# Optimization experiments

Hardware: AMD Instinct MI355X
Metric: run time of the kernel (lower is better)

Reference implementation:

```python
import jax, jax.numpy as jnp
import numpy as np

W_KERNEL = 5      # dilation kernel size (w)
K_BG = 0.1        # background weight (k)
RELAX = 5.0       # sigmoid temperature (relax)
INF = 1e4         # 'no zero in column' sentinel (>> image diagonal)
EPS = 1e-7        # DiceLoss eps


def setup_inputs() -> dict:
    key = jax.random.key(0)
    k1, k2 = jax.random.split(key)
    B, H, W = 32, 256, 256
    preds = jax.random.normal(k1, (B, H, W), dtype=jnp.float32)
    targets = (jax.random.uniform(k2, (B, H, W)) > 0.99).astype(jnp.float32)
    return {"preds": preds, "targets": targets}


def _dilate(t, w):
    # cv2.dilate with w x w ones kernel == sliding-window max, SAME padding
    pad = w // 2
    return jax.lax.reduce_window(t, -jnp.inf, jax.lax.max,
                                 (1, w, w), (1, 1, 1),
                                 [(0, 0), (pad, pad), (pad, pad)])


def _vertical_dist(zero_mask):
    # per-column distance (in rows) to nearest zero pixel; [B,H,W] -> [B,H,W]
    B, H, W = zero_mask.shape
    rows = jnp.moveaxis(zero_mask, 1, 0)  # [H,B,W]

    def step(carry, z):
        d = jnp.where(z, 0.0, jnp.minimum(carry + 1.0, INF))
        return d, d

    init = jnp.full((B, W), INF, dtype=jnp.float32)
    _, fwd = jax.lax.scan(step, init, rows)
    _, bwd = jax.lax.scan(step, init, rows[::-1])
    g = jnp.minimum(fwd, bwd[::-1])  # [H,B,W]
    return jnp.moveaxis(g, 0, 1)


def _edt(fat):
    # exact euclidean distance transform (distance to nearest zero pixel),
    # separable two-pass: vertical 1D distance, then horizontal min-plus.
    B, H, W = fat.shape
    g = _vertical_dist(fat == 0)  # [B,H,W]
    col = jnp.arange(W, dtype=jnp.float32)
    off2 = (col[:, None] - col[None, :]) ** 2  # [W_j, W_k]

    def per_img(gi):  # gi: [H,W]
        # d2[i,j] = min_k g[i,k]^2 + (j-k)^2   -> [H,W,W] intermediate
        d2 = jnp.min(gi[:, None, :] ** 2 + off2[None, :, :], axis=-1)
        return jnp.sqrt(d2)

    return jax.lax.map(per_img, g)  # sequential over batch caps memory


def _distance_maps(targets):
    fat = _dilate(targets, W_KERNEL)          # [B,H,W]
    d = _edt(fat)                              # [B,H,W]
    soft = jax.nn.sigmoid(d / RELAX)
    soft = soft - jnp.min(soft, axis=(1, 2), keepdims=True)
    mx = jnp.max(soft, axis=(1, 2), keepdims=True)
    soft = soft / jnp.where(mx > 0, mx, 1.0)
    dm_soft = soft + (1.0 - fat) * K_BG
    has_fg = jnp.max(targets, axis=(1, 2), keepdims=True) > 0
    return jnp.where(has_fg, dm_soft, 1.0 - targets)


def reference(preds, targets):
    p = jax.nn.sigmoid(preds)
    dm = jax.lax.stop_gradient(_distance_maps(targets))  # computed in numpy in torch => constant
    pw = p * dm
    bs = pw.shape[0]
    y_pred = pw.reshape(bs, 1, -1)
    y_true = targets.reshape(bs, 1, -1)
    # smp DiceLoss('binary', from_logits=False): dims=(0,2), smooth=0, eps=1e-7
    inter = jnp.sum(y_pred * y_true, axis=(0, 2))
    card = jnp.sum(y_pred + y_true, axis=(0, 2))
    dice = (2.0 * inter) / jnp.maximum(card, EPS)
    loss = 1.0 - dice
    mask = (jnp.sum(y_true, axis=(0, 2)) > 0).astype(loss.dtype)
    return jnp.mean(loss * mask)
```

## Files before the change

kernel.cpp:

```cpp
#include <hip/hip_runtime.h>
#include <math.h>

#define BB 32
#define HH 256
#define WW 256
#define HW (HH*WW)
#define K_BG 0.1f
#define RELAX 5.0f
#define EPS_D 1e-7
#define RPB 8

typedef unsigned long long u64;
typedef unsigned short u16;

__device__ __forceinline__ float sigf(float x) { return 1.0f / (1.0f + expf(-x)); }

__device__ __forceinline__ u64 shflx64(u64 x, int s) {
    return (u64)__shfl_xor((unsigned long long)x, s, 64);
}

__global__ void k_maskdil(const float* __restrict__ tg, u64* __restrict__ dmaskT,
                          u64* __restrict__ nzmask) {
    __shared__ u64 nz[20][4];
    __shared__ u64 hd[20][4];
    int blk = blockIdx.x;
    int b = blk >> 4, band = blk & 15;
    int r0 = band * 16;
    int t = threadIdx.x, w = t >> 6;
    const float* img = tg + b * HW;
    float v[20];
    #pragma unroll
    for (int rr = 0; rr < 20; ++rr) {
        int rg = r0 + rr - 2;
        v[rr] = (rg >= 0 && rg < HH) ? img[rg * WW + t] : 0.0f;
    }
    #pragma unroll
    for (int rr = 0; rr < 20; ++rr) {
        u64 bal = __ballot(v[rr] != 0.0f);
        if ((t & 63) == 0) nz[rr][w] = bal;
    }
    __syncthreads();
    if (t < 80) {
        int rr = t >> 2, k = t & 3;
        u64 m = nz[rr][k];
        u64 ml = (k > 0) ? nz[rr][k - 1] : 0ULL;
        u64 mr = (k < 3) ? nz[rr][k + 1] : 0ULL;
        hd[rr][k] = m | (m << 1) | (m << 2) | (m >> 1) | (m >> 2)
                  | (ml >> 62) | (ml >> 63) | (mr << 62) | (mr << 63);
    }
    if (t < 64) {
        int rr = t >> 2, k = t & 3;
        nzmask[b * 1024 + (r0 + rr) * 4 + k] = nz[rr + 2][k];
    }
    __syncthreads();
    if (t < 64) {
        int rr = t >> 2, k = t & 3;
        u64 o = hd[rr][k] | hd[rr + 1][k] | hd[rr + 2][k] | hd[rr + 3][k] | hd[rr + 4][k];
        dmaskT[b * 1024 + k * 256 + (r0 + rr)] = o;
    }
}

__global__ __launch_bounds__(256) void k_mega(const float* __restrict__ preds,
                                              const u64* __restrict__ dmaskT,
                                              const u64* __restrict__ nzmask,
                                              float4* __restrict__ part1,
                                              float4* __restrict__ part2) {
    __shared__ u64 colT[4 * 256];
    __shared__ u16 gS[RPB][WW];
    __shared__ float red[8][4];
    int blk = blockIdx.x;
    int b = blk >> 5, q = blk & 31;
    int i0 = q * RPB;
    int tid = threadIdx.x;
    int lane = tid & 63, wv = tid >> 6;
    int j = tid;

    float p[RPB];
    #pragma unroll
    for (int rr = 0; rr < RPB; ++rr)
        p[rr] = preds[(b * HH + i0 + rr) * WW + j];
    u64 nzw[RPB];
    #pragma unroll
    for (int rr = 0; rr < RPB; ++rr)
        nzw[rr] = nzmask[b * 1024 + (i0 + rr) * 4 + wv];

    const u64* base = dmaskT + b * 1024;
    const u64 L32 = 0x00000000FFFFFFFFULL, L16 = 0x0000FFFF0000FFFFULL,
              L8  = 0x00FF00FF00FF00FFULL, L4  = 0x0F0F0F0F0F0F0F0FULL,
              L2  = 0x3333333333333333ULL, L1  = 0x5555555555555555ULL;
    #pragma unroll
    for (int w = 0; w < 4; ++w) {
        u64 x = base[w * 256 + wv * 64 + lane];
        u64 pp;
        pp = shflx64(x, 32); x = (lane & 32) ? ((x & ~L32) | ((pp & ~L32) >> 32)) : ((x & L32) | ((pp & L32) << 32));
        pp = shflx64(x, 16); x = (lane & 16) ? ((x & ~L16) | ((pp & ~L16) >> 16)) : ((x & L16) | ((pp & L16) << 16));
        pp = shflx64(x,  8); x = (lane &  8) ? ((x & ~L8 ) | ((pp & ~L8 ) >>  8)) : ((x & L8 ) | ((pp & L8 ) <<  8));
        pp = shflx64(x,  4); x = (lane &  4) ? ((x & ~L4 ) | ((pp & ~L4 ) >>  4)) : ((x & L4 ) | ((pp & L4 ) <<  4));
        pp = shflx64(x,  2); x = (lane &  2) ? ((x & ~L2 ) | ((pp & ~L2 ) >>  2)) : ((x & L2 ) | ((pp & L2 ) <<  2));
        pp = shflx64(x,  1); x = (lane &  1) ? ((x & ~L1 ) | ((pp & ~L1 ) >>  1)) : ((x & L1 ) | ((pp & L1 ) <<  1));
        colT[wv * 256 + w * 64 + lane] = x;
    }
    __syncthreads();

    u64 yw[4];
    #pragma unroll
    for (int g = 0; g < 4; ++g) yw[g] = ~colT[g * 256 + j];

    int g0v[RPB], fgv[RPB];
    #pragma unroll
    for (int rr = 0; rr < RPB; ++rr) {
        int i = i0 + rr;
        int iw = i >> 6, ib = i & 63;
        u64 lowm  = (2ULL << ib) - 1ULL;
        u64 highm = ~((1ULL << ib) - 1ULL);
        int pu = -1, pd = -1;
        #pragma unroll
        for (int w = 0; w < 4; ++w) {
            u64 m = (w < iw) ? ~0ULL : ((w == iw) ? lowm : 0ULL);
            u64 z = yw[w] & m;
            int cand = (w << 6) + 63 - __clzll(z);
            pu = z ? cand : pu;
        }
        #pragma unroll
        for (int w = 3; w >= 0; --w) {
            u64 m = (w > iw) ? ~0ULL : ((w == iw) ? highm : 0ULL);
            u64 z = yw[w] & m;
            int cand = (w << 6) + (__ffsll((unsigned long long)z) - 1);
            pd = z ? cand : pd;
        }
        int up = (pu >= 0) ? (i - pu) : 10000;
        int dn = (pd >= 0) ? (pd - i) : 10000;
        int g0 = min(min(up, dn), 10000);
        g0v[rr] = g0;
        fgv[rr] = (int)((~yw[iw] >> ib) & 1ULL);
        gS[rr][j] = (u16)g0;
    }
    __syncthreads();

    float vals[8];
    #pragma unroll
    for (int qq = 0; qq < 6; ++qq) vals[qq] = 0.0f;
    vals[6] = 1e30f; vals[7] = 0.0f;
    #pragma unroll
    for (int rr = 0; rr < RPB; ++rr) {
        float gv = (float)g0v[rr];
        float best = gv * gv;
        #pragma unroll
        for (int r = 1; r <= 8; ++r) {
            float rf = (float)(r * r);
            int jl = j - r, jr = j + r;
            float vl = (jl >= 0) ? (float)gS[rr][jl] : 1e4f;
            float vr = (jr < WW) ? (float)gS[rr][jr] : 1e4f;
            best = fminf(best, fminf(fmaf(vl, vl, rf), fmaf(vr, vr, rf)));
        }
        for (int rc = 9; rc < WW + 8; rc += 8) {
            if ((float)(rc * rc) >= best) break;
            #pragma unroll
            for (int dr = 0; dr < 8; ++dr) {
                int r = rc + dr;
                float rf = (float)(r * r);
                int jl = j - r, jr = j + r;
                float vl = (jl >= 0) ? (float)gS[rr][jl] : 1e4f;
                float vr = (jr < WW) ? (float)gS[rr][jr] : 1e4f;
                best = fminf(best, fminf(fmaf(vl, vl, rf), fmaf(vr, vr, rf)));
            }
        }
        float dv = sqrtf(best);
        float sp = sigf(p[rr]);
        float sd = sigf(dv / RELAX);
        float tv = (float)((nzw[rr] >> (j & 63)) & 1ULL);
        vals[0] += sp * sd * tv;
        vals[1] += sp * tv;
        vals[2] += sp * sd;
        vals[3] += sp;
        vals[4] += fgv[rr] ? 0.0f : sp;
        vals[5] += tv;
        vals[6] = fminf(vals[6], dv);
        vals[7] = fmaxf(vals[7], dv);
    }
    for (int off = 32; off > 0; off >>= 1) {
        #pragma unroll
        for (int qq = 0; qq < 6; ++qq) vals[qq] += __shfl_down(vals[qq], off, 64);
        vals[6] = fminf(vals[6], __shfl_down(vals[6], off, 64));
        vals[7] = fmaxf(vals[7], __shfl_down(vals[7], off, 64));
    }
    if (lane == 0) {
        #pragma unroll
        for (int qq = 0; qq < 8; ++qq) red[qq][wv] = vals[qq];
    }
    __syncthreads();
    if (tid == 0) {
        float s[8];
        #pragma unroll
        for (int qq = 0; qq < 6; ++qq) s[qq] = red[qq][0] + red[qq][1] + red[qq][2] + red[qq][3];
        s[6] = fminf(fminf(red[6][0], red[6][1]), fminf(red[6][2], red[6][3]));
        s[7] = fmaxf(fmaxf(red[7][0], red[7][1]), fmaxf(red[7][2], red[7][3]));
        part1[blk] = make_float4(s[0], s[1], s[2], s[3]);
        part2[blk] = make_float4(s[4], s[5], s[6], s[7]);
    }
}

__global__ void k_tail(const float4* __restrict__ part1, const float4* __restrict__ part2,
                       float* __restrict__ out) {
    __shared__ float sI[32], sC[32], sA[32];
    int t = threadIdx.x;
    #pragma unroll
    for (int pass = 0; pass < 4; ++pass) {
        int img = pass * 8 + (t >> 5);
        int k = t & 31;
        float4 p1 = part1[img * 32 + k];
        float4 p2 = part2[img * 32 + k];
        float vals[8] = {p1.x, p1.y, p1.z, p1.w, p2.x, p2.y, p2.z, p2.w};
        for (int off = 16; off > 0; off >>= 1) {
            #pragma unroll
            for (int qq = 0; qq < 6; ++qq) vals[qq] += __shfl_down(vals[qq], off, 32);
            vals[6] = fminf(vals[6], __shfl_down(vals[6], off, 32));
            vals[7] = fmaxf(vals[7], __shfl_down(vals[7], off, 32));
        }
        if (k == 0) {
            float A = vals[0], Bs = vals[1], Ap = vals[2], Bp = vals[3];
            float Cp = vals[4], T = vals[5], dmn = vals[6], dmx = vals[7];
            float inter, card, any;
            if (dmx > 0.0f) {
                float smin = sigf(dmn / RELAX);
                float smax = sigf(dmx / RELAX);
                float m = smax - smin;
                float denom = (m > 0.0f) ? m : 1.0f;
                inter = (A - smin * Bs) / denom;
                card  = (Ap - smin * Bp) / denom + K_BG * Cp + T;
                any = 1.0f;
            } else {
                inter = 0.0f;
                card = Bp - Bs + T;
                any = 0.0f;
            }
            sI[img] = inter; sC[img] = card; sA[img] = any;
        }
    }
    __syncthreads();
    if (t == 0) {
        double I = 0.0, C = 0.0;
        int any = 0;
        for (int b = 0; b < BB; ++b) {
            I += (double)sI[b]; C += (double)sC[b];
            any |= (sA[b] > 0.0f);
        }
        double dice = 2.0 * I / fmax(C, (double)EPS_D);
        out[0] = any ? (float)(1.0 - dice) : 0.0f;
    }
}

extern "C" void kernel_launch(void* const* d_in, const int* in_sizes, int n_in,
                              void* d_out, int out_size, void* d_ws, size_t ws_size,
                              hipStream_t stream) {
    const float* preds = (const float*)d_in[0];
    const float* tg    = (const float*)d_in[1];
    float* out = (float*)d_out;

    u64* dmaskT   = (u64*)d_ws;
    u64* nzmask   = dmaskT + BB * 1024;
    float4* part1 = (float4*)(nzmask + BB * 1024);
    float4* part2 = part1 + BB * 32;

    hipLaunchKernelGGL(k_maskdil, dim3(BB * 16), dim3(WW), 0, stream, tg, dmaskT, nzmask);
    hipLaunchKernelGGL(k_mega, dim3(BB * 32), dim3(WW), 0, stream, preds, dmaskT, nzmask,
                       part1, part2);
    hipLaunchKernelGGL(k_tail, dim3(1), dim3(256), 0, stream, part1, part2, out);
}
```

Before: 93.32 us.

## Move column bit-transpose into mask kernel and fuse tail via last-block atomic

```diff
diff --git a/kernel.cpp b/kernel.cpp
--- a/kernel.cpp
+++ b/kernel.cpp
@@ -8,10 +8,10 @@
 #define K_BG 0.1f
 #define RELAX 5.0f
 #define EPS_D 1e-7
-#define RPB 8
+#define RPB 4
+#define MEGA_BLOCKS (BB * (HH / RPB))
 
 typedef unsigned long long u64;
-typedef unsigned short u16;
 
 __device__ __forceinline__ float sigf(float x) { return 1.0f / (1.0f + expf(-x)); }
 
@@ -19,78 +19,65 @@
     return (u64)__shfl_xor((unsigned long long)x, s, 64);
 }
 
-__global__ void k_maskdil(const float* __restrict__ tg, u64* __restrict__ dmaskT,
-                          u64* __restrict__ nzmask) {
-    __shared__ u64 nz[20][4];
-    __shared__ u64 hd[20][4];
+__global__ __launch_bounds__(512) void k_maskdil(const float* __restrict__ tg,
+                                                 u64* __restrict__ colmask,
+                                                 u64* __restrict__ nzmask,
+                                                 unsigned* __restrict__ cnt) {
+    __shared__ u64 nz[68][4];
+    __shared__ u64 hd[68][4];
+    __shared__ u64 dil[64][5];
     int blk = blockIdx.x;
-    int b = blk >> 4, band = blk & 15;
-    int r0 = band * 16;
-    int t = threadIdx.x, w = t >> 6;
+    int b = blk >> 2, g = blk & 3;
+    int r0 = g * 64;
+    int tid = threadIdx.x;
+    int col = tid & 255;
+    int team = tid >> 8;
     const float* img = tg + b * HW;
-    float v[20];
-    #pragma unroll
-    for (int rr = 0; rr < 20; ++rr) {
-        int rg = r0 + rr - 2;
-        v[rr] = (rg >= 0 && rg < HH) ? img[rg * WW + t] : 0.0f;
-    }
-    #pragma unroll
-    for (int rr = 0; rr < 20; ++rr) {
-        u64 bal = __ballot(v[rr] != 0.0f);
-        if ((t & 63) == 0) nz[rr][w] = bal;
-    }
-    __syncthreads();
-    if (t < 80) {
-        int rr = t >> 2, k = t & 3;
-        u64 m = nz[rr][k];
-        u64 ml = (k > 0) ? nz[rr][k - 1] : 0ULL;
-        u64 mr = (k < 3) ? nz[rr][k + 1] : 0ULL;
-        hd[rr][k] = m | (m << 1) | (m << 2) | (m >> 1) | (m >> 2)
+    if (blk == 0 && tid == 0) cnt[0] = 0;
+
+    const int RT = 34;
+    int lr0 = team * RT;
+    for (int base = 0; base < RT; base += 12) {
+        float v[12];
+        #pragma unroll
+        for (int k = 0; k < 12; ++k) {
+            int lr = lr0 + base + k;
+            int rg = r0 - 2 + lr;
+            v[k] = (base + k < RT && rg >= 0 && rg < HH) ? img[rg * WW + col] : 0.0f;
+        }
+        #pragma unroll
+        for (int k = 0; k < 12; ++k) {
+            if (base + k < RT) {
+                u64 bal = __ballot(v[k] != 0.0f);
+                if ((tid & 63) == 0) nz[lr0 + base + k][(tid >> 6) & 3] = bal;
+            }
+        }
+    }
+    __syncthreads();
+    if (tid < 272) {
+        int lr = tid >> 2, k = tid & 3;
+        u64 m = nz[lr][k];
+        u64 ml = (k > 0) ? nz[lr][k - 1] : 0ULL;
+        u64 mr = (k < 3) ? nz[lr][k + 1] : 0ULL;
+        hd[lr][k] = m | (m << 1) | (m << 2) | (m >> 1) | (m >> 2)
                   | (ml >> 62) | (ml >> 63) | (mr << 62) | (mr << 63);
     }
-    if (t < 64) {
-        int rr = t >> 2, k = t & 3;
+    if (tid < 256) {
+        int rr = tid >> 2, k = tid & 3;
         nzmask[b * 1024 + (r0 + rr) * 4 + k] = nz[rr + 2][k];
     }
     __syncthreads();
-    if (t < 64) {
-        int rr = t >> 2, k = t & 3;
-        u64 o = hd[rr][k] | hd[rr + 1][k] | hd[rr + 2][k] | hd[rr + 3][k] | hd[rr + 4][k];
-        dmaskT[b * 1024 + k * 256 + (r0 + rr)] = o;
-    }
-}
-
-__global__ __launch_bounds__(256) void k_mega(const float* __restrict__ preds,
-                                              const u64* __restrict__ dmaskT,
-                                              const u64* __restrict__ nzmask,
-                                              float4* __restrict__ part1,
-                                              float4* __restrict__ part2) {
-    __shared__ u64 colT[4 * 256];
-    __shared__ u16 gS[RPB][WW];
-    __shared__ float red[8][4];
-    int blk = blockIdx.x;
-    int b = blk >> 5, q = blk & 31;
-    int i0 = q * RPB;
-    int tid = threadIdx.x;
-    int lane = tid & 63, wv = tid >> 6;
-    int j = tid;
-
-    float p[RPB];
-    #pragma unroll
-    for (int rr = 0; rr < RPB; ++rr)
-        p[rr] = preds[(b * HH + i0 + rr) * WW + j];
-    u64 nzw[RPB];
-    #pragma unroll
-    for (int rr = 0; rr < RPB; ++rr)
-        nzw[rr] = nzmask[b * 1024 + (i0 + rr) * 4 + wv];
-
-    const u64* base = dmaskT + b * 1024;
-    const u64 L32 = 0x00000000FFFFFFFFULL, L16 = 0x0000FFFF0000FFFFULL,
-              L8  = 0x00FF00FF00FF00FFULL, L4  = 0x0F0F0F0F0F0F0F0FULL,
-              L2  = 0x3333333333333333ULL, L1  = 0x5555555555555555ULL;
-    #pragma unroll
-    for (int w = 0; w < 4; ++w) {
-        u64 x = base[w * 256 + wv * 64 + lane];
+    if (tid < 256) {
+        int rr = tid >> 2, k = tid & 3;
+        dil[rr][k] = hd[rr][k] | hd[rr + 1][k] | hd[rr + 2][k] | hd[rr + 3][k] | hd[rr + 4][k];
+    }
+    __syncthreads();
+    if (tid < 256) {
+        int w = tid >> 6, lane = tid & 63;
+        u64 x = dil[lane][w];
+        const u64 L32 = 0x00000000FFFFFFFFULL, L16 = 0x0000FFFF0000FFFFULL,
+                  L8  = 0x00FF00FF00FF00FFULL, L4  = 0x0F0F0F0F0F0F0F0FULL,
+                  L2  = 0x3333333333333333ULL, L1  = 0x5555555555555555ULL;
         u64 pp;
         pp = shflx64(x, 32); x = (lane & 32) ? ((x & ~L32) | ((pp & ~L32) >> 32)) : ((x & L32) | ((pp & L32) << 32));
         pp = shflx64(x, 16); x = (lane & 16) ? ((x & ~L16) | ((pp & ~L16) >> 16)) : ((x & L16) | ((pp & L16) << 16));
@@ -98,13 +85,40 @@
         pp = shflx64(x,  4); x = (lane &  4) ? ((x & ~L4 ) | ((pp & ~L4 ) >>  4)) : ((x & L4 ) | ((pp & L4 ) <<  4));
         pp = shflx64(x,  2); x = (lane &  2) ? ((x & ~L2 ) | ((pp & ~L2 ) >>  2)) : ((x & L2 ) | ((pp & L2 ) <<  2));
         pp = shflx64(x,  1); x = (lane &  1) ? ((x & ~L1 ) | ((pp & ~L1 ) >>  1)) : ((x & L1 ) | ((pp & L1 ) <<  1));
-        colT[wv * 256 + w * 64 + lane] = x;
-    }
-    __syncthreads();
-
+        colmask[b * 1024 + g * 256 + w * 64 + lane] = x;
+    }
+}
+
+__global__ __launch_bounds__(256, 8) void k_mega(const float* __restrict__ preds,
+                                                 const u64* __restrict__ colmask,
+                                                 const u64* __restrict__ nzmask,
+                                                 float4* __restrict__ part1,
+                                                 float4* __restrict__ part2,
+                                                 unsigned* __restrict__ cnt,
+                                                 float* __restrict__ out) {
+    __shared__ float gS[RPB][WW];
+    __shared__ float red[8][4];
+    __shared__ unsigned stick;
+    __shared__ float sI[BB], sC[BB], sA[BB];
+    int blk = blockIdx.x;
+    int b = blk >> 6, q = blk & 63;
+    int i0 = q * RPB;
+    int tid = threadIdx.x;
+    int lane = tid & 63, wv = tid >> 6;
+    int j = tid;
+
+    float p[RPB];
+    #pragma unroll
+    for (int rr = 0; rr < RPB; ++rr)
+        p[rr] = preds[(b * HH + i0 + rr) * WW + j];
+    u64 nzw[RPB];
+    #pragma unroll
+    for (int rr = 0; rr < RPB; ++rr)
+        nzw[rr] = nzmask[b * 1024 + (i0 + rr) * 4 + wv];
     u64 yw[4];
     #pragma unroll
-    for (int g = 0; g < 4; ++g) yw[g] = ~colT[g * 256 + j];
+    for (int g = 0; g < 4; ++g)
+        yw[g] = ~colmask[b * 1024 + g * 256 + j];
 
     int g0v[RPB], fgv[RPB];
     #pragma unroll
@@ -133,7 +147,7 @@
         int g0 = min(min(up, dn), 10000);
         g0v[rr] = g0;
         fgv[rr] = (int)((~yw[iw] >> ib) & 1ULL);
-        gS[rr][j] = (u16)g0;
+        gS[rr][j] = (float)g0;
     }
     __syncthreads();
 
@@ -149,8 +163,8 @@
         for (int r = 1; r <= 8; ++r) {
             float rf = (float)(r * r);
             int jl = j - r, jr = j + r;
-            float vl = (jl >= 0) ? (float)gS[rr][jl] : 1e4f;
-            float vr = (jr < WW) ? (float)gS[rr][jr] : 1e4f;
+            float vl = (jl >= 0) ? gS[rr][jl] : 1e4f;
+            float vr = (jr < WW) ? gS[rr][jr] : 1e4f;
             best = fminf(best, fminf(fmaf(vl, vl, rf), fmaf(vr, vr, rf)));
         }
         for (int rc = 9; rc < WW + 8; rc += 8) {
@@ -160,8 +174,8 @@
                 int r = rc + dr;
                 float rf = (float)(r * r);
                 int jl = j - r, jr = j + r;
-                float vl = (jl >= 0) ? (float)gS[rr][jl] : 1e4f;
-                float vr = (jr < WW) ? (float)gS[rr][jr] : 1e4f;
+                float vl = (jl >= 0) ? gS[rr][jl] : 1e4f;
+                float vr = (jr < WW) ? gS[rr][jr] : 1e4f;
                 best = fminf(best, fminf(fmaf(vl, vl, rf), fmaf(vr, vr, rf)));
             }
         }
@@ -197,29 +211,28 @@
         s[7] = fmaxf(fmaxf(red[7][0], red[7][1]), fmaxf(red[7][2], red[7][3]));
         part1[blk] = make_float4(s[0], s[1], s[2], s[3]);
         part2[blk] = make_float4(s[4], s[5], s[6], s[7]);
-    }
-}
-
-__global__ void k_tail(const float4* __restrict__ part1, const float4* __restrict__ part2,
-                       float* __restrict__ out) {
-    __shared__ float sI[32], sC[32], sA[32];
-    int t = threadIdx.x;
-    #pragma unroll
-    for (int pass = 0; pass < 4; ++pass) {
-        int img = pass * 8 + (t >> 5);
-        int k = t & 31;
-        float4 p1 = part1[img * 32 + k];
-        float4 p2 = part2[img * 32 + k];
-        float vals[8] = {p1.x, p1.y, p1.z, p1.w, p2.x, p2.y, p2.z, p2.w};
-        for (int off = 16; off > 0; off >>= 1) {
+        __threadfence();
+        stick = atomicAdd(cnt, 1u);
+    }
+    __syncthreads();
+    if (stick != MEGA_BLOCKS - 1) return;
+
+    __threadfence();
+    #pragma unroll
+    for (int pass = 0; pass < 8; ++pass) {
+        int img = pass * 4 + wv;
+        float4 p1 = part1[img * 64 + lane];
+        float4 p2 = part2[img * 64 + lane];
+        float v2[8] = {p1.x, p1.y, p1.z, p1.w, p2.x, p2.y, p2.z, p2.w};
+        for (int off = 32; off > 0; off >>= 1) {
             #pragma unroll
-            for (int qq = 0; qq < 6; ++qq) vals[qq] += __shfl_down(vals[qq], off, 32);
-            vals[6] = fminf(vals[6], __shfl_down(vals[6], off, 32));
-            vals[7] = fmaxf(vals[7], __shfl_down(vals[7], off, 32));
-        }
-        if (k == 0) {
-            float A = vals[0], Bs = vals[1], Ap = vals[2], Bp = vals[3];
-            float Cp = vals[4], T = vals[5], dmn = vals[6], dmx = vals[7];
+            for (int qq = 0; qq < 6; ++qq) v2[qq] += __shfl_down(v2[qq], off, 64);
+            v2[6] = fminf(v2[6], __shfl_down(v2[6], off, 64));
+            v2[7] = fmaxf(v2[7], __shfl_down(v2[7], off, 64));
+        }
+        if (lane == 0) {
+            float A = v2[0], Bs = v2[1], Ap = v2[2], Bp = v2[3];
+            float Cp = v2[4], T = v2[5], dmn = v2[6], dmx = v2[7];
             float inter, card, any;
             if (dmx > 0.0f) {
                 float smin = sigf(dmn / RELAX);
@@ -238,12 +251,12 @@
         }
     }
     __syncthreads();
-    if (t == 0) {
+    if (tid == 0) {
         double I = 0.0, C = 0.0;
         int any = 0;
-        for (int b = 0; b < BB; ++b) {
-            I += (double)sI[b]; C += (double)sC[b];
-            any |= (sA[b] > 0.0f);
+        for (int bb = 0; bb < BB; ++bb) {
+            I += (double)sI[bb]; C += (double)sC[bb];
+            any |= (sA[bb] > 0.0f);
         }
         double dice = 2.0 * I / fmax(C, (double)EPS_D);
         out[0] = any ? (float)(1.0 - dice) : 0.0f;
@@ -257,13 +270,14 @@
     const float* tg    = (const float*)d_in[1];
     float* out = (float*)d_out;
 
-    u64* dmaskT   = (u64*)d_ws;
-    u64* nzmask   = dmaskT + BB * 1024;
+    u64* colmask  = (u64*)d_ws;
+    u64* nzmask   = colmask + BB * 1024;
     float4* part1 = (float4*)(nzmask + BB * 1024);
-    float4* part2 = part1 + BB * 32;
-
-    hipLaunchKernelGGL(k_maskdil, dim3(BB * 16), dim3(WW), 0, stream, tg, dmaskT, nzmask);
-    hipLaunchKernelGGL(k_mega, dim3(BB * 32), dim3(WW), 0, stream, preds, dmaskT, nzmask,
-                       part1, part2);
-    hipLaunchKernelGGL(k_tail, dim3(1), dim3(256), 0, stream, part1, part2, out);
-}
+    float4* part2 = part1 + MEGA_BLOCKS;
+    unsigned* cnt = (unsigned*)(part2 + MEGA_BLOCKS);
+
+    hipLaunchKernelGGL(k_maskdil, dim3(BB * 4), dim3(512), 0, stream,
+                       tg, colmask, nzmask, cnt);
+    hipLaunchKernelGGL(k_mega, dim3(MEGA_BLOCKS), dim3(WW), 0, stream,
+                       preds, colmask, nzmask, part1, part2, cnt, out);
+}
```

Measured after the change: 130.4 us. 1.4x slower.

## Fuse tail reduction into main kernel via last-block atomic and interleave min-plus rows

Applied to the files above, without the earlier changes.

```diff
diff --git a/kernel.cpp b/kernel.cpp
--- a/kernel.cpp
+++ b/kernel.cpp
@@ -9,9 +9,9 @@
 #define RELAX 5.0f
 #define EPS_D 1e-7
 #define RPB 8
+#define MEGA_BLOCKS (BB * (HH / RPB))
 
 typedef unsigned long long u64;
-typedef unsigned short u16;
 
 __device__ __forceinline__ float sigf(float x) { return 1.0f / (1.0f + expf(-x)); }
 
@@ -20,7 +20,7 @@
 }
 
 __global__ void k_maskdil(const float* __restrict__ tg, u64* __restrict__ dmaskT,
-                          u64* __restrict__ nzmask) {
+                          u64* __restrict__ nzmask, unsigned* __restrict__ cnt) {
     __shared__ u64 nz[20][4];
     __shared__ u64 hd[20][4];
     int blk = blockIdx.x;
@@ -28,6 +28,7 @@
     int r0 = band * 16;
     int t = threadIdx.x, w = t >> 6;
     const float* img = tg + b * HW;
+    if (blk == 0 && t == 0) cnt[0] = 0;
     float v[20];
     #pragma unroll
     for (int rr = 0; rr < 20; ++rr) {
@@ -60,14 +61,18 @@
     }
 }
 
-__global__ __launch_bounds__(256) void k_mega(const float* __restrict__ preds,
-                                              const u64* __restrict__ dmaskT,
-                                              const u64* __restrict__ nzmask,
-                                              float4* __restrict__ part1,
-                                              float4* __restrict__ part2) {
+__global__ __launch_bounds__(256, 4) void k_mega(const float* __restrict__ preds,
+                                                 const u64* __restrict__ dmaskT,
+                                                 const u64* __restrict__ nzmask,
+                                                 float4* __restrict__ part1,
+                                                 float4* __restrict__ part2,
+                                                 unsigned* __restrict__ cnt,
+                                                 float* __restrict__ out) {
     __shared__ u64 colT[4 * 256];
-    __shared__ u16 gS[RPB][WW];
+    __shared__ float gS[RPB][WW];
     __shared__ float red[8][4];
+    __shared__ unsigned stick;
+    __shared__ float sI[BB], sC[BB], sA[BB];
     int blk = blockIdx.x;
     int b = blk >> 5, q = blk & 31;
     int i0 = q * RPB;
@@ -133,39 +138,51 @@
         int g0 = min(min(up, dn), 10000);
         g0v[rr] = g0;
         fgv[rr] = (int)((~yw[iw] >> ib) & 1ULL);
-        gS[rr][j] = (u16)g0;
-    }
-    __syncthreads();
-
-    float vals[8];
-    #pragma unroll
-    for (int qq = 0; qq < 6; ++qq) vals[qq] = 0.0f;
-    vals[6] = 1e30f; vals[7] = 0.0f;
+        gS[rr][j] = (float)g0;
+    }
+    __syncthreads();
+
+    float best[RPB];
     #pragma unroll
     for (int rr = 0; rr < RPB; ++rr) {
         float gv = (float)g0v[rr];
-        float best = gv * gv;
-        #pragma unroll
-        for (int r = 1; r <= 8; ++r) {
-            float rf = (float)(r * r);
-            int jl = j - r, jr = j + r;
-            float vl = (jl >= 0) ? (float)gS[rr][jl] : 1e4f;
-            float vr = (jr < WW) ? (float)gS[rr][jr] : 1e4f;
-            best = fminf(best, fminf(fmaf(vl, vl, rf), fmaf(vr, vr, rf)));
-        }
+        best[rr] = gv * gv;
+    }
+    #pragma unroll
+    for (int r = 1; r <= 8; ++r) {
+        float rf = (float)(r * r);
+        int jl = j - r, jr = j + r;
+        bool okl = (jl >= 0), okr = (jr < WW);
+        #pragma unroll
+        for (int rr = 0; rr < RPB; ++rr) {
+            float vl = okl ? gS[rr][jl] : 1e4f;
+            float vr = okr ? gS[rr][jr] : 1e4f;
+            best[rr] = fminf(best[rr], fminf(fmaf(vl, vl, rf), fmaf(vr, vr, rf)));
+        }
+    }
+    #pragma unroll
+    for (int rr = 0; rr < RPB; ++rr) {
         for (int rc = 9; rc < WW + 8; rc += 8) {
-            if ((float)(rc * rc) >= best) break;
+            if ((float)(rc * rc) >= best[rr]) break;
             #pragma unroll
             for (int dr = 0; dr < 8; ++dr) {
                 int r = rc + dr;
                 float rf = (float)(r * r);
                 int jl = j - r, jr = j + r;
-                float vl = (jl >= 0) ? (float)gS[rr][jl] : 1e4f;
-                float vr = (jr < WW) ? (float)gS[rr][jr] : 1e4f;
-                best = fminf(best, fminf(fmaf(vl, vl, rf), fmaf(vr, vr, rf)));
+                float vl = (jl >= 0) ? gS[rr][jl] : 1e4f;
+                float vr = (jr < WW) ? gS[rr][jr] : 1e4f;
+                best[rr] = fminf(best[rr], fminf(fmaf(vl, vl, rf), fmaf(vr, vr, rf)));
             }
         }
-        float dv = sqrtf(best);
+    }
+
+    float vals[8];
+    #pragma unroll
+    for (int qq = 0; qq < 6; ++qq) vals[qq] = 0.0f;
+    vals[6] = 1e30f; vals[7] = 0.0f;
+    #pragma unroll
+    for (int rr = 0; rr < RPB; ++rr) {
+        float dv = sqrtf(best[rr]);
         float sp = sigf(p[rr]);
         float sd = sigf(dv / RELAX);
         float tv = (float)((nzw[rr] >> (j & 63)) & 1ULL);
@@ -197,29 +214,29 @@
         s[7] = fmaxf(fmaxf(red[7][0], red[7][1]), fmaxf(red[7][2], red[7][3]));
         part1[blk] = make_float4(s[0], s[1], s[2], s[3]);
         part2[blk] = make_float4(s[4], s[5], s[6], s[7]);
-    }
-}
-
-__global__ void k_tail(const float4* __restrict__ part1, const float4* __restrict__ part2,
-                       float* __restrict__ out) {
-    __shared__ float sI[32], sC[32], sA[32];
-    int t = threadIdx.x;
+        __threadfence();
+        stick = atomicAdd(cnt, 1u);
+    }
+    __syncthreads();
+    if (stick != MEGA_BLOCKS - 1) return;
+
+    __threadfence();
     #pragma unroll
     for (int pass = 0; pass < 4; ++pass) {
-        int img = pass * 8 + (t >> 5);
-        int k = t & 31;
+        int img = pass * 8 + (tid >> 5);
+        int k = tid & 31;
         float4 p1 = part1[img * 32 + k];
         float4 p2 = part2[img * 32 + k];
-        float vals[8] = {p1.x, p1.y, p1.z, p1.w, p2.x, p2.y, p2.z, p2.w};
+        float v2[8] = {p1.x, p1.y, p1.z, p1.w, p2.x, p2.y, p2.z, p2.w};
         for (int off = 16; off > 0; off >>= 1) {
             #pragma unroll
-            for (int qq = 0; qq < 6; ++qq) vals[qq] += __shfl_down(vals[qq], off, 32);
-            vals[6] = fminf(vals[6], __shfl_down(vals[6], off, 32));
-            vals[7] = fmaxf(vals[7], __shfl_down(vals[7], off, 32));
+            for (int qq = 0; qq < 6; ++qq) v2[qq] += __shfl_down(v2[qq], off, 32);
+            v2[6] = fminf(v2[6], __shfl_down(v2[6], off, 32));
+            v2[7] = fmaxf(v2[7], __shfl_down(v2[7], off, 32));
         }
         if (k == 0) {
-            float A = vals[0], Bs = vals[1], Ap = vals[2], Bp = vals[3];
-            float Cp = vals[4], T = vals[5], dmn = vals[6], dmx = vals[7];
+            float A = v2[0], Bs = v2[1], Ap = v2[2], Bp = v2[3];
+            float Cp = v2[4], T = v2[5], dmn = v2[6], dmx = v2[7];
             float inter, card, any;
             if (dmx > 0.0f) {
                 float smin = sigf(dmn / RELAX);
@@ -238,12 +255,12 @@
         }
     }
     __syncthreads();
-    if (t == 0) {
+    if (tid == 0) {
         double I = 0.0, C = 0.0;
         int any = 0;
-        for (int b = 0; b < BB; ++b) {
-            I += (double)sI[b]; C += (double)sC[b];
-            any |= (sA[b] > 0.0f);
+        for (int bb = 0; bb < BB; ++bb) {
+            I += (double)sI[bb]; C += (double)sC[bb];
+            any |= (sA[bb] > 0.0f);
         }
         double dice = 2.0 * I / fmax(C, (double)EPS_D);
         out[0] = any ? (float)(1.0 - dice) : 0.0f;
@@ -260,10 +277,11 @@
     u64* dmaskT   = (u64*)d_ws;
     u64* nzmask   = dmaskT + BB * 1024;
     float4* part1 = (float4*)(nzmask + BB * 1024);
-    float4* part2 = part1 + BB * 32;
-
-    hipLaunchKernelGGL(k_maskdil, dim3(BB * 16), dim3(WW), 0, stream, tg, dmaskT, nzmask);
-    hipLaunchKernelGGL(k_mega, dim3(BB * 32), dim3(WW), 0, stream, preds, dmaskT, nzmask,
-                       part1, part2);
-    hipLaunchKernelGGL(k_tail, dim3(1), dim3(256), 0, stream, part1, part2, out);
-}
+    float4* part2 = part1 + MEGA_BLOCKS;
+    unsigned* cnt = (unsigned*)(part2 + MEGA_BLOCKS);
+
+    hipLaunchKernelGGL(k_maskdil, dim3(BB * 16), dim3(WW), 0, stream,
+                       tg, dmaskT, nzmask, cnt);
+    hipLaunchKernelGGL(k_mega, dim3(MEGA_BLOCKS), dim3(WW), 0, stream,
+                       preds, dmaskT, nzmask, part1, part2, cnt, out);
+}
```

Measured after the change: 127.9 us. 1.37x slower.
